# Performance work log

Hardware: AMD Instinct MI355X
Metric: run time of the kernel (lower is better)

## Reference

```python
import jax, jax.numpy as jnp
import numpy as np

B, K, H, W = 16, 64, 28, 28
HID, OUT = 128, 128
FLAT = 64 * 4 * 4  # 28 -> (28-5)//2+1=12 -> (12-5)//2+1=4 after two 5x5 stride-2 VALID convs


def setup_inputs() -> dict:
    key = jax.random.key(0)
    ks = jax.random.split(key, 12)
    g = lambda k, shape, s=0.05: jax.random.normal(k, shape, dtype=jnp.float32) * s
    return {
        "x": jax.random.normal(ks[0], (B, K, H, W), dtype=jnp.float32),
        "conv1_w": g(ks[1], (32, 1, 5, 5)),
        "conv1_b": g(ks[2], (32,)),
        "conv2_w": g(ks[3], (64, 32, 5, 5)),
        "conv2_b": g(ks[4], (64,)),
        "fc_w": g(ks[5], (HID, FLAT)),
        "fc_b": g(ks[6], (HID,)),
        "coeffs": g(ks[7], (HID, OUT, 15), float(np.sqrt(2.0 / (HID + OUT)))),
        "eq_bias": g(ks[8], (OUT,)),
        "diag_bias": g(ks[9], (OUT,)),
        "out_w": g(ks[10], (1, OUT)),
        "out_b": g(ks[11], (1,)),
    }


def _conv(x, w, b, stride):
    y = jax.lax.conv_general_dilated(x, w, (stride, stride), 'VALID',
                                     dimension_numbers=('NCHW', 'OIHW', 'NCHW'))
    return y + b[None, :, None, None]


def _ops_2_to_2(P):
    # P: (B, D, m, m) -> (B, D, 15, m, m), Maron et al. basis, 'inf' normalization
    m = P.shape[-1]
    mf = jnp.asarray(m, P.dtype)
    I = jnp.eye(m, dtype=P.dtype)
    diag = jnp.diagonal(P, axis1=-2, axis2=-1)            # (B,D,m)
    sum_diag = diag.sum(-1, keepdims=True)                # (B,D,1)
    sum_rows = P.sum(-1)                                  # (B,D,m)
    sum_cols = P.sum(-2)                                  # (B,D,m)
    sum_all = P.sum((-2, -1))[..., None, None]            # (B,D,1,1)
    de = lambda v: v[..., None] * I                       # diag_embed
    bc = lambda v: jnp.broadcast_to(v, P.shape)
    op1 = de(diag)
    op2 = de(jnp.broadcast_to(sum_diag, diag.shape)) / mf
    op3 = de(sum_rows) / mf
    op4 = de(sum_cols) / mf
    op5 = de(jnp.broadcast_to(sum_all[..., 0], diag.shape)) / (mf * mf)
    op6 = bc(sum_cols[..., :, None]) / mf
    op7 = bc(sum_rows[..., :, None]) / mf
    op8 = bc(sum_cols[..., None, :]) / mf
    op9 = bc(sum_rows[..., None, :]) / mf
    op10 = P
    op11 = jnp.swapaxes(P, -1, -2)
    op12 = bc(diag[..., :, None])
    op13 = bc(diag[..., None, :])
    op14 = bc(sum_diag[..., None]) / mf
    op15 = bc(sum_all) / (mf * mf)
    return jnp.stack([op1, op2, op3, op4, op5, op6, op7, op8,
                      op9, op10, op11, op12, op13, op14, op15], axis=2)


def reference(x, conv1_w, conv1_b, conv2_w, conv2_b, fc_w, fc_b,
              coeffs, eq_bias, diag_bias, out_w, out_b):
    Bx, k, h, w = x.shape
    y = x.reshape(Bx * k, 1, h, w)
    y = jax.nn.relu(_conv(y, conv1_w, conv1_b, 2))
    y = jax.nn.relu(_conv(y, conv2_w, conv2_b, 2))
    y = y.reshape(Bx * k, -1) @ fc_w.T + fc_b              # (B*k, HID)
    feat = y.reshape(Bx, k, -1)                            # (B, k, D)
    P = jnp.einsum('bid,bjd->bdij', feat, feat)            # (B, D, k, k)
    ops = _ops_2_to_2(P)                                   # (B, D, 15, k, k)
    out = jnp.einsum('dsp,bdpij->bsij', coeffs, ops)       # (B, S, k, k)
    out = out + eq_bias[None, :, None, None]
    out = out + jnp.eye(k, dtype=out.dtype) * diag_bias[None, :, None, None]
    out = jax.nn.relu(out).mean((-2, -1))                  # (B, S)
    out = jax.nn.relu(out)                                 # dropout_prob=0 / eval: identity
    return out @ out_w.T + out_b                           # (B, 1)
```

## Files before the change

### kernel.cpp

```cpp
#include <hip/hip_runtime.h>


#define FS_IDX(r, d) (((r) << 7) + (((((d) >> 2) ^ (((r) >> 2) & 7))) << 2) + ((d) & 3))

__global__ __launch_bounds__(256) void k_prep(
        const float* __restrict__ coeffs, const float* __restrict__ fc_w,
        const float* __restrict__ w2,
        float* __restrict__ CaT,  float* __restrict__ CdgT, float* __restrict__ CdrT,
        float* __restrict__ CugT, float* __restrict__ CurT,
        float* __restrict__ CvgT, float* __restrict__ CvrT,
        float* __restrict__ CctT, float* __restrict__ CcAT,
        float* __restrict__ CwtT, float* __restrict__ CwAT,
        float* __restrict__ fcwT, float* __restrict__ w2R,
        float* __restrict__ dout) {
    int idx = blockIdx.x * 256 + threadIdx.x;
    if (idx < 16384) {
        int d = idx >> 7, s = idx & 127;
        const float* c = coeffs + idx * 15;
        const float im = 1.0f / 64.0f, im2 = 1.0f / 4096.0f;
        int t = s * 128 + d;
        CaT[t]  = c[9] + c[10];
        CdgT[t] = c[0];
        CdrT[t] = (c[2] + c[3]) * im;
        CurT[t] = (c[5] + c[6]) * im;
        CugT[t] = c[11];
        CvrT[t] = (c[7] + c[8]) * im;
        CvgT[t] = c[12];
        CctT[t] = c[1] * im;
        CcAT[t] = c[4] * im2;
        CwtT[t] = c[13] * im;
        CwAT[t] = c[14] * im2;
        if (idx < 16) dout[idx] = 0.0f;
    } else if (idx < 147456) {
        int e = idx - 16384;
        int s = e >> 10, k = e & 1023;
        fcwT[k * 128 + s] = fc_w[e];
    } else if (idx < 198656) {
        int e = idx - 147456;
        int ic = e & 31;
        int q = e >> 5;
        int kx = q % 5, q2 = q / 5, ky = q2 % 5, oc = q2 / 5;
        w2R[e] = w2[oc * 800 + ic * 25 + ky * 5 + kx];
    }
}

__global__ __launch_bounds__(256, 2) void k_convfc(
        const float* __restrict__ x,  const float* __restrict__ w1,
        const float* __restrict__ b1, const float* __restrict__ w2R,
        const float* __restrict__ b2, const float* __restrict__ fcwT,
        const float* __restrict__ fc_b, float* __restrict__ feat) {
    __shared__ alignas(16) float xs[1568];
    __shared__ alignas(16) float w1s[800];
    __shared__ alignas(16) float c1T[4608];
    __shared__ alignas(16) float ysh[2][1024];
    __shared__ alignas(16) float ps[8][2][128];
    int tid = threadIdx.x;
    int n0 = blockIdx.x * 2;

    {
        const float4* xsrc = (const float4*)(x + n0 * 784);
        float4* xdst = (float4*)xs;
        for (int i = tid; i < 392; i += 256) xdst[i] = xsrc[i];
        const float4* wsrc = (const float4*)w1;
        float4* wdst = (float4*)w1s;
        for (int i = tid; i < 200; i += 256) wdst[i] = wsrc[i];
    }
    __syncthreads();

    for (int img = 0; img < 2; ++img) {
        for (int task = tid; task < 384; task += 256) {
            int oy = task >> 5, oc = task & 31;
            const float* wp = w1s + oc * 25;
            float wr[25];
#pragma unroll
            for (int t = 0; t < 25; ++t) wr[t] = wp[t];
            float out[12];
            float bv = b1[oc];
#pragma unroll
            for (int ox = 0; ox < 12; ++ox) out[ox] = bv;
            const float* xb = xs + img * 784 + (oy * 2) * 28;
#pragma unroll
            for (int ky = 0; ky < 5; ++ky) {
                const float4* rp = (const float4*)(xb + ky * 28);
                float4 r0 = rp[0], r1 = rp[1], r2 = rp[2], r3 = rp[3];
                float4 r4 = rp[4], r5 = rp[5], r6 = rp[6];
                float rf[28] = {r0.x, r0.y, r0.z, r0.w, r1.x, r1.y, r1.z, r1.w,
                                r2.x, r2.y, r2.z, r2.w, r3.x, r3.y, r3.z, r3.w,
                                r4.x, r4.y, r4.z, r4.w, r5.x, r5.y, r5.z, r5.w,
                                r6.x, r6.y, r6.z, r6.w};
#pragma unroll
                for (int kx = 0; kx < 5; ++kx) {
                    float wv = wr[ky * 5 + kx];
#pragma unroll
                    for (int ox = 0; ox < 12; ++ox)
                        out[ox] = fmaf(rf[2 * ox + kx], wv, out[ox]);
                }
            }
#pragma unroll
            for (int ox = 0; ox < 12; ++ox)
                c1T[(oy * 12 + ox) * 32 + oc] = fmaxf(out[ox], 0.0f);
        }
        __syncthreads();

        {
            int icg = tid & 7, ocg = tid >> 3;
            int ic0 = icg * 4;
            float acc[2][16];
#pragma unroll
            for (int l = 0; l < 2; ++l)
#pragma unroll
                for (int p = 0; p < 16; ++p) acc[l][p] = 0.0f;
#pragma unroll
            for (int ky = 0; ky < 5; ++ky) {
                float4 wv[2][5];
#pragma unroll
                for (int l = 0; l < 2; ++l) {
                    int oc = ocg * 2 + l;
#pragma unroll
                    for (int kx = 0; kx < 5; ++kx)
                        wv[l][kx] = *(const float4*)&w2R[((oc * 5 + ky) * 5 + kx) * 32 + ic0];
                }
#pragma unroll
                for (int oyy = 0; oyy < 4; ++oyy) {
                    int y = 2 * oyy + ky;
                    float4 v[12];
#pragma unroll
                    for (int xx = 0; xx < 12; ++xx)
                        v[xx] = *(const float4*)&c1T[(y * 12 + xx) * 32 + ic0];
#pragma unroll
                    for (int l = 0; l < 2; ++l)
#pragma unroll
                        for (int ox = 0; ox < 4; ++ox) {
                            float s = acc[l][oyy * 4 + ox];
#pragma unroll
                            for (int kx = 0; kx < 5; ++kx) {
                                float4 vv = v[2 * ox + kx];
                                float4 ww = wv[l][kx];
                                s = fmaf(vv.x, ww.x, s);
                                s = fmaf(vv.y, ww.y, s);
                                s = fmaf(vv.z, ww.z, s);
                                s = fmaf(vv.w, ww.w, s);
                            }
                            acc[l][oyy * 4 + ox] = s;
                        }
                }
            }
#pragma unroll
            for (int m = 1; m < 8; m <<= 1)
#pragma unroll
                for (int l = 0; l < 2; ++l)
#pragma unroll
                    for (int p = 0; p < 16; ++p)
                        acc[l][p] += __shfl_xor(acc[l][p], m);
            if (icg == 0) {
#pragma unroll
                for (int l = 0; l < 2; ++l) {
                    int oc = ocg * 2 + l;
                    float bb = b2[oc];
#pragma unroll
                    for (int p = 0; p < 16; ++p)
                        ysh[img][oc * 16 + p] = fmaxf(acc[l][p] + bb, 0.0f);
                }
            }
        }
        __syncthreads();
    }

    {
        int sg = tid & 31, kc = tid >> 5;
        const float* yb0 = &ysh[0][kc * 128];
        const float* yb1 = &ysh[1][kc * 128];
        const float* wb = fcwT + kc * 128 * 128 + sg * 4;
        float4 a0 = {0.f, 0.f, 0.f, 0.f}, a1 = {0.f, 0.f, 0.f, 0.f};
#pragma unroll 4
        for (int i = 0; i < 128; ++i) {
            float4 w = *(const float4*)(wb + i * 128);
            float y0 = yb0[i], y1 = yb1[i];
            a0.x = fmaf(y0, w.x, a0.x); a0.y = fmaf(y0, w.y, a0.y);
            a0.z = fmaf(y0, w.z, a0.z); a0.w = fmaf(y0, w.w, a0.w);
            a1.x = fmaf(y1, w.x, a1.x); a1.y = fmaf(y1, w.y, a1.y);
            a1.z = fmaf(y1, w.z, a1.z); a1.w = fmaf(y1, w.w, a1.w);
        }
        *(float4*)&ps[kc][0][sg * 4] = a0;
        *(float4*)&ps[kc][1][sg * 4] = a1;
    }
    __syncthreads();
    {
        int img = tid >> 7, s = tid & 127;
        float acc = fc_b[s];
#pragma unroll
        for (int kc = 0; kc < 8; ++kc) acc += ps[kc][img][s];
        feat[(n0 + img) * 128 + s] = acc;
    }
}

__global__ __launch_bounds__(256, 2) void k_main2(
        const float* __restrict__ feat,
        const float* __restrict__ CaT,  const float* __restrict__ CdgT,
        const float* __restrict__ CdrT, const float* __restrict__ CugT,
        const float* __restrict__ CurT, const float* __restrict__ CvgT,
        const float* __restrict__ CvrT, const float* __restrict__ CctT,
        const float* __restrict__ CcAT, const float* __restrict__ CwtT,
        const float* __restrict__ CwAT,
        const float* __restrict__ eq_bias, const float* __restrict__ diag_bias,
        const float* __restrict__ out_w,   const float* __restrict__ out_b,
        float* __restrict__ dout) {
    __shared__ alignas(16) float fs[8192];
    __shared__ alignas(16) float ash2[512];
    __shared__ alignas(16) float Ssh[128];
    __shared__ float Uv[4][64], Vv[4][64], Dv[4][64];
    __shared__ float parts[2][8];
    __shared__ float red[4][4];
    int b = blockIdx.x >> 5, sq = blockIdx.x & 31;
    int s0 = sq * 4;
    int tid = threadIdx.x;
    const float* fb = feat + b * 8192;

    for (int i = tid; i < 8192; i += 256) {
        int r = i >> 7, d = i & 127;
        fs[FS_IDX(r, d)] = fb[i];
    }
    for (int i = tid; i < 512; i += 256) {
        int d = i >> 2, sl = i & 3;
        ash2[d * 4 + sl] = CaT[(s0 + sl) * 128 + d];
    }
    __syncthreads();

    if (tid < 128) {
        int d = tid;
        float sv = 0.f, tv = 0.f;
        for (int r = 0; r < 64; ++r) {
            float v = fs[FS_IDX(r, d)];
            sv += v;
            tv = fmaf(v, v, tv);
        }
        Ssh[d] = sv;
        float av = sv * sv;
        float dc[4], wv[4];
#pragma unroll
        for (int sl = 0; sl < 4; ++sl) {
            int o = (s0 + sl) * 128 + d;
            dc[sl] = fmaf(CctT[o], tv, CcAT[o] * av);
            wv[sl] = fmaf(CwtT[o], tv, CwAT[o] * av);
        }
#pragma unroll
        for (int m = 1; m < 64; m <<= 1)
#pragma unroll
            for (int sl = 0; sl < 4; ++sl) {
                dc[sl] += __shfl_xor(dc[sl], m);
                wv[sl] += __shfl_xor(wv[sl], m);
            }
        if ((tid & 63) == 0) {
            int w = tid >> 6;
#pragma unroll
            for (int sl = 0; sl < 4; ++sl) {
                parts[w][sl] = dc[sl];
                parts[w][4 + sl] = wv[sl];
            }
        }
    }
    __syncthreads();

    int tx = tid & 15, ty = tid >> 4;
    {
        int d0 = tx * 8;
        float4 s0v = *(const float4*)&Ssh[d0];
        float4 s1v = *(const float4*)&Ssh[d0 + 4];
        float sv[8] = {s0v.x, s0v.y, s0v.z, s0v.w, s1v.x, s1v.y, s1v.z, s1v.w};
#pragma unroll
        for (int sl = 0; sl < 4; ++sl) {
            int o = (s0 + sl) * 128 + d0;
            float4 A0, A1;
#define LD8(arr, p) A0 = *(const float4*)&arr[o]; A1 = *(const float4*)&arr[o + 4]; \
            float p[8] = {A0.x, A0.y, A0.z, A0.w, A1.x, A1.y, A1.z, A1.w};
            LD8(CdgT, cg) LD8(CdrT, cr) LD8(CugT, ug) LD8(CurT, ur) LD8(CvgT, vg) LD8(CvrT, vr)
#undef LD8
            float pD[4], pU[4], pV[4];
#pragma unroll
            for (int u = 0; u < 4; ++u) {
                int i = ty * 4 + u;
                float4 fA = *(const float4*)&fs[FS_IDX(i, d0)];
                float4 fB = *(const float4*)&fs[FS_IDX(i, d0 + 4)];
                float fv[8] = {fA.x, fA.y, fA.z, fA.w, fB.x, fB.y, fB.z, fB.w};
                float aD = 0.f, aU = 0.f, aV = 0.f;
#pragma unroll
                for (int e = 0; e < 8; ++e) {
                    float g = fv[e] * fv[e];
                    float rr = fv[e] * sv[e];
                    aD = fmaf(cg[e], g, fmaf(cr[e], rr, aD));
                    aU = fmaf(ug[e], g, fmaf(ur[e], rr, aU));
                    aV = fmaf(vg[e], g, fmaf(vr[e], rr, aV));
                }
                pD[u] = aD; pU[u] = aU; pV[u] = aV;
            }
#pragma unroll
            for (int m = 1; m < 16; m <<= 1)
#pragma unroll
                for (int u = 0; u < 4; ++u) {
                    pD[u] += __shfl_xor(pD[u], m);
                    pU[u] += __shfl_xor(pU[u], m);
                    pV[u] += __shfl_xor(pV[u], m);
                }
            if (tx == 0)
#pragma unroll
                for (int u = 0; u < 4; ++u) {
                    Dv[sl][ty * 4 + u] = pD[u];
                    Uv[sl][ty * 4 + u] = pU[u];
                    Vv[sl][ty * 4 + u] = pV[u];
                }
        }
    }
    __syncthreads();

    float acc[4][16];
#pragma unroll
    for (int sl = 0; sl < 4; ++sl)
#pragma unroll
        for (int q = 0; q < 16; ++q) acc[sl][q] = 0.f;
    for (int d = 0; d < 128; d += 4) {
        float aif[4][4], bjf[4][4], a4f[4][4];
#pragma unroll
        for (int u = 0; u < 4; ++u) {
            float4 t = *(const float4*)&fs[FS_IDX(ty * 4 + u, d)];
            aif[u][0] = t.x; aif[u][1] = t.y; aif[u][2] = t.z; aif[u][3] = t.w;
        }
#pragma unroll
        for (int v = 0; v < 4; ++v) {
            float4 t = *(const float4*)&fs[FS_IDX(tx * 4 + v, d)];
            bjf[v][0] = t.x; bjf[v][1] = t.y; bjf[v][2] = t.z; bjf[v][3] = t.w;
        }
#pragma unroll
        for (int dd = 0; dd < 4; ++dd) {
            float4 t = *(const float4*)&ash2[(d + dd) * 4];
            a4f[dd][0] = t.x; a4f[dd][1] = t.y; a4f[dd][2] = t.z; a4f[dd][3] = t.w;
        }
#pragma unroll
        for (int dd = 0; dd < 4; ++dd)
#pragma unroll
            for (int sl = 0; sl < 4; ++sl)
#pragma unroll
                for (int u = 0; u < 4; ++u) {
                    float t = aif[u][dd] * a4f[dd][sl];
#pragma unroll
                    for (int v = 0; v < 4; ++v)
                        acc[sl][u * 4 + v] = fmaf(t, bjf[v][dd], acc[sl][u * 4 + v]);
                }
    }

    float sDc[4], sW[4];
#pragma unroll
    for (int sl = 0; sl < 4; ++sl) {
        sDc[sl] = parts[0][sl] + parts[1][sl] + diag_bias[s0 + sl];
        sW[sl]  = parts[0][4 + sl] + parts[1][4 + sl] + eq_bias[s0 + sl];
    }
    float psum[4] = {0.f, 0.f, 0.f, 0.f};
#pragma unroll
    for (int u = 0; u < 4; ++u) {
        int i = ty * 4 + u;
#pragma unroll
        for (int v = 0; v < 4; ++v) {
            int j = tx * 4 + v;
#pragma unroll
            for (int sl = 0; sl < 4; ++sl) {
                float val = acc[sl][u * 4 + v] + Uv[sl][i] + Vv[sl][j] + sW[sl];
                if (i == j) val += Dv[sl][i] + sDc[sl];
                psum[sl] += fmaxf(val, 0.0f);
            }
        }
    }
#pragma unroll
    for (int m = 1; m < 64; m <<= 1)
#pragma unroll
        for (int sl = 0; sl < 4; ++sl) psum[sl] += __shfl_xor(psum[sl], m);
    if ((tid & 63) == 0) {
        int w = tid >> 6;
#pragma unroll
        for (int sl = 0; sl < 4; ++sl) red[w][sl] = psum[sl];
    }
    __syncthreads();
    if (tid == 0) {
        float o = 0.f;
#pragma unroll
        for (int sl = 0; sl < 4; ++sl) {
            float tot = red[0][sl] + red[1][sl] + red[2][sl] + red[3][sl];
            o += fmaxf(tot * (1.0f / 4096.0f), 0.0f) * out_w[s0 + sl];
        }
        if (s0 == 0) o += out_b[0];
        atomicAdd(dout + b, o);
    }
}

extern "C" void kernel_launch(void* const* d_in, const int* in_sizes, int n_in,
                              void* d_out, int out_size, void* d_ws, size_t ws_size,
                              hipStream_t stream) {
    const float* x      = (const float*)d_in[0];
    const float* w1     = (const float*)d_in[1];
    const float* b1     = (const float*)d_in[2];
    const float* w2     = (const float*)d_in[3];
    const float* b2     = (const float*)d_in[4];
    const float* fc_w   = (const float*)d_in[5];
    const float* fc_b   = (const float*)d_in[6];
    const float* coeffs = (const float*)d_in[7];
    const float* eqb    = (const float*)d_in[8];
    const float* dgb    = (const float*)d_in[9];
    const float* out_w  = (const float*)d_in[10];
    const float* out_b  = (const float*)d_in[11];

    float* ws = (float*)d_ws;
    float* feat = ws; ws += 131072;
    float* fcwT = ws; ws += 131072;
    float* w2R  = ws; ws += 51200;
    float* CaT  = ws; ws += 16384;
    float* CdgT = ws; ws += 16384;
    float* CdrT = ws; ws += 16384;
    float* CugT = ws; ws += 16384;
    float* CurT = ws; ws += 16384;
    float* CvgT = ws; ws += 16384;
    float* CvrT = ws; ws += 16384;
    float* CctT = ws; ws += 16384;
    float* CcAT = ws; ws += 16384;
    float* CwtT = ws; ws += 16384;
    float* CwAT = ws; ws += 16384;

    k_prep<<<776, 256, 0, stream>>>(coeffs, fc_w, w2,
                                    CaT, CdgT, CdrT, CugT, CurT, CvgT, CvrT,
                                    CctT, CcAT, CwtT, CwAT, fcwT, w2R,
                                    (float*)d_out);
    k_convfc<<<512, 256, 0, stream>>>(x, w1, b1, w2R, b2, fcwT, fc_b, feat);
    k_main2<<<512, 256, 0, stream>>>(feat, CaT, CdgT, CdrT, CugT, CurT,
                                     CvgT, CvrT, CctT, CcAT, CwtT, CwAT,
                                     eqb, dgb, out_w, out_b, (float*)d_out);
}
```

Measured before the change: 206.5 us.

## Remap conv2 threads to one output channel with 8-channel slices and padded smem

```diff
diff --git a/kernel.cpp b/kernel.cpp
--- a/kernel.cpp
+++ b/kernel.cpp
@@ -44,14 +44,14 @@
     }
 }
 
-__global__ __launch_bounds__(256, 2) void k_convfc(
+__global__ __launch_bounds__(256) void k_convfc(
         const float* __restrict__ x,  const float* __restrict__ w1,
         const float* __restrict__ b1, const float* __restrict__ w2R,
         const float* __restrict__ b2, const float* __restrict__ fcwT,
         const float* __restrict__ fc_b, float* __restrict__ feat) {
     __shared__ alignas(16) float xs[1568];
     __shared__ alignas(16) float w1s[800];
-    __shared__ alignas(16) float c1T[4608];
+    __shared__ alignas(16) float c1T[144 * 36];
     __shared__ alignas(16) float ysh[2][1024];
     __shared__ alignas(16) float ps[8][2][128];
     int tid = threadIdx.x;
@@ -98,69 +98,62 @@
             }
 #pragma unroll
             for (int ox = 0; ox < 12; ++ox)
-                c1T[(oy * 12 + ox) * 32 + oc] = fmaxf(out[ox], 0.0f);
+                c1T[(oy * 12 + ox) * 36 + oc] = fmaxf(out[ox], 0.0f);
         }
         __syncthreads();
 
         {
-            int icg = tid & 7, ocg = tid >> 3;
-            int ic0 = icg * 4;
-            float acc[2][16];
-#pragma unroll
-            for (int l = 0; l < 2; ++l)
-#pragma unroll
-                for (int p = 0; p < 16; ++p) acc[l][p] = 0.0f;
-#pragma unroll
+            int icg = tid & 3, oc = tid >> 2;
+            int ic0 = icg * 8;
+            float acc[16];
+#pragma unroll
+            for (int p = 0; p < 16; ++p) acc[p] = 0.0f;
             for (int ky = 0; ky < 5; ++ky) {
-                float4 wv[2][5];
-#pragma unroll
-                for (int l = 0; l < 2; ++l) {
-                    int oc = ocg * 2 + l;
-#pragma unroll
-                    for (int kx = 0; kx < 5; ++kx)
-                        wv[l][kx] = *(const float4*)&w2R[((oc * 5 + ky) * 5 + kx) * 32 + ic0];
+                float4 wv[5][2];
+#pragma unroll
+                for (int kx = 0; kx < 5; ++kx) {
+                    const float* wb = &w2R[((oc * 5 + ky) * 5 + kx) * 32 + ic0];
+                    wv[kx][0] = *(const float4*)(wb);
+                    wv[kx][1] = *(const float4*)(wb + 4);
                 }
 #pragma unroll
                 for (int oyy = 0; oyy < 4; ++oyy) {
                     int y = 2 * oyy + ky;
-                    float4 v[12];
-#pragma unroll
-                    for (int xx = 0; xx < 12; ++xx)
-                        v[xx] = *(const float4*)&c1T[(y * 12 + xx) * 32 + ic0];
-#pragma unroll
-                    for (int l = 0; l < 2; ++l)
+                    const float* rowb = c1T + (y * 12) * 36 + ic0;
+#pragma unroll
+                    for (int xx = 0; xx < 12; ++xx) {
+                        float4 v0 = *(const float4*)(rowb + xx * 36);
+                        float4 v1 = *(const float4*)(rowb + xx * 36 + 4);
 #pragma unroll
                         for (int ox = 0; ox < 4; ++ox) {
-                            float s = acc[l][oyy * 4 + ox];
-#pragma unroll
-                            for (int kx = 0; kx < 5; ++kx) {
-                                float4 vv = v[2 * ox + kx];
-                                float4 ww = wv[l][kx];
-                                s = fmaf(vv.x, ww.x, s);
-                                s = fmaf(vv.y, ww.y, s);
-                                s = fmaf(vv.z, ww.z, s);
-                                s = fmaf(vv.w, ww.w, s);
+                            int kx = xx - 2 * ox;
+                            if (kx >= 0 && kx < 5) {
+                                float4 w0 = wv[kx][0], w1v = wv[kx][1];
+                                float s = acc[oyy * 4 + ox];
+                                s = fmaf(v0.x, w0.x, s);
+                                s = fmaf(v0.y, w0.y, s);
+                                s = fmaf(v0.z, w0.z, s);
+                                s = fmaf(v0.w, w0.w, s);
+                                s = fmaf(v1.x, w1v.x, s);
+                                s = fmaf(v1.y, w1v.y, s);
+                                s = fmaf(v1.z, w1v.z, s);
+                                s = fmaf(v1.w, w1v.w, s);
+                                acc[oyy * 4 + ox] = s;
                             }
-                            acc[l][oyy * 4 + ox] = s;
                         }
-                }
-            }
-#pragma unroll
-            for (int m = 1; m < 8; m <<= 1)
-#pragma unroll
-                for (int l = 0; l < 2; ++l)
-#pragma unroll
-                    for (int p = 0; p < 16; ++p)
-                        acc[l][p] += __shfl_xor(acc[l][p], m);
+                    }
+                }
+            }
+#pragma unroll
+            for (int m = 1; m < 4; m <<= 1)
+#pragma unroll
+                for (int p = 0; p < 16; ++p)
+                    acc[p] += __shfl_xor(acc[p], m);
             if (icg == 0) {
-#pragma unroll
-                for (int l = 0; l < 2; ++l) {
-                    int oc = ocg * 2 + l;
-                    float bb = b2[oc];
-#pragma unroll
-                    for (int p = 0; p < 16; ++p)
-                        ysh[img][oc * 16 + p] = fmaxf(acc[l][p] + bb, 0.0f);
-                }
+                float bb = b2[oc];
+#pragma unroll
+                for (int p = 0; p < 16; ++p)
+                    ysh[img][oc * 16 + p] = fmaxf(acc[p] + bb, 0.0f);
             }
         }
         __syncthreads();
@@ -194,7 +187,7 @@
     }
 }
 
-__global__ __launch_bounds__(256, 2) void k_main2(
+__global__ __launch_bounds__(256) void k_main2(
         const float* __restrict__ feat,
         const float* __restrict__ CaT,  const float* __restrict__ CdgT,
         const float* __restrict__ CdrT, const float* __restrict__ CugT,
```

Result: faster. 173.4 us (-16.0%).
